# Performance work log

Hardware: AMD Instinct MI355X
Metric: run time of the kernel (lower is better)

Reference implementation:

```python
import jax, jax.numpy as jnp
import numpy as np

N_TOK = 16384   # total tokens (batch*seq)
H = 2048        # hidden_size
I = 768         # moe_intermediate_size (per-expert MLP width)
TOPK = 8        # num_experts_per_tok


def setup_inputs() -> dict:
    key = jax.random.key(0)
    ks = jax.random.split(key, 7)
    hidden_states = jax.random.normal(ks[0], (N_TOK, H), dtype=jnp.float32)
    # expert_mask[j, k] != 0 means token k selected this expert at top-k slot j
    expert_mask = jax.random.randint(ks[1], (TOPK, N_TOK), 0, 2, dtype=jnp.int32)
    routing_weights = jax.random.uniform(ks[2], (N_TOK, TOPK), dtype=jnp.float32)
    final_hidden_states = jax.random.normal(ks[3], (N_TOK, H), dtype=jnp.float32)
    gate_w = jax.random.normal(ks[4], (I, H), dtype=jnp.float32) * 0.02
    up_w = jax.random.normal(ks[5], (I, H), dtype=jnp.float32) * 0.02
    down_w = jax.random.normal(ks[6], (H, I), dtype=jnp.float32) * 0.02
    return {
        "hidden_states": hidden_states,
        "expert_mask": expert_mask,
        "routing_weights": routing_weights,
        "final_hidden_states": final_hidden_states,
        "gate_w": gate_w,
        "up_w": up_w,
        "down_w": down_w,
    }


def reference(hidden_states, expert_mask, routing_weights, final_hidden_states,
              gate_w, up_w, down_w):
    # forward_expert: gather selected tokens, SwiGLU MLP, scale by routing weight,
    # scatter-add into final_hidden_states. Equivalent jit-friendly form: the
    # combined routing weight per token is w[k] = sum_j mask[j,k]*routing_weights[k,j]
    # (tokens selected multiple times are summed, matching index_add_ semantics),
    # and unselected tokens get w[k]=0 so they contribute nothing.
    g = hidden_states @ gate_w.T                       # [N, I]
    u = hidden_states @ up_w.T                         # [N, I]
    y = (jax.nn.silu(g) * u) @ down_w.T                # [N, H]
    w = jnp.einsum('jk,kj->k', expert_mask.astype(y.dtype), routing_weights)  # [N]
    return final_hidden_states + y * w[:, None]
```

## Files before the change

### kernel.cpp

```cpp
#include <hip/hip_runtime.h>
#include <stdint.h>

#define NTOK 16384
#define HD   2048
#define ID   768
#define TOPK 8

typedef __bf16 bf16x8 __attribute__((ext_vector_type(8)));
typedef float  floatx4 __attribute__((ext_vector_type(4)));
typedef unsigned short ushort8 __attribute__((ext_vector_type(8)));

__device__ __forceinline__ unsigned short f32_to_bf16_rne(float f) {
    union { float f; uint32_t u; } v; v.f = f;
    uint32_t u = v.u;
    u += 0x7FFFu + ((u >> 16) & 1u);
    return (unsigned short)(u >> 16);
}
__device__ __forceinline__ float bf16_to_f32(unsigned short h) {
    union { uint32_t u; float f; } v; v.u = ((uint32_t)h) << 16;
    return v.f;
}

#define GLD_LDS(gsrc, ldst)                                                              \
    __builtin_amdgcn_global_load_lds(                                                    \
        (const __attribute__((address_space(1))) uint32_t*)(const void*)(gsrc),          \
        (__attribute__((address_space(3))) uint32_t*)(void*)(ldst), 16, 0, 0)

template<int VM> __device__ __forceinline__ void wait_vm() {
    if constexpr (VM == 4)      asm volatile("s_waitcnt vmcnt(4)" ::: "memory");
    else                        asm volatile("s_waitcnt vmcnt(0)" ::: "memory");
}
#define BARRIER() do { asm volatile("" ::: "memory");              \
                       __builtin_amdgcn_s_barrier();               \
                       asm volatile("" ::: "memory"); } while (0)

__global__ __launch_bounds__(256) void compute_w_kernel(const int* __restrict__ mask,
                                                        const float* __restrict__ rw,
                                                        float* __restrict__ w) {
    int k = blockIdx.x * 256 + threadIdx.x;
    if (k >= NTOK) return;
    float acc = 0.f;
#pragma unroll
    for (int j = 0; j < TOPK; ++j)
        acc += (float)mask[j * NTOK + k] * rw[k * TOPK + j];
    w[k] = acc;
}

__global__ __launch_bounds__(256) void convert_hs_kernel(const float* __restrict__ src,
                                                         unsigned short* __restrict__ dst) {
    size_t i = (size_t)blockIdx.x * 256 + threadIdx.x;
    const float4* s = (const float4*)src;
    float4 a = s[2 * i], b = s[2 * i + 1];
    ushort8 o;
    o[0] = f32_to_bf16_rne(a.x); o[1] = f32_to_bf16_rne(a.y);
    o[2] = f32_to_bf16_rne(a.z); o[3] = f32_to_bf16_rne(a.w);
    o[4] = f32_to_bf16_rne(b.x); o[5] = f32_to_bf16_rne(b.y);
    o[6] = f32_to_bf16_rne(b.z); o[7] = f32_to_bf16_rne(b.w);
    *(ushort8*)(dst + 8 * i) = o;
}

__global__ __launch_bounds__(256) void convert_w3_kernel(const float* __restrict__ g,
                                                         const float* __restrict__ u,
                                                         const float* __restrict__ d,
                                                         unsigned short* __restrict__ dst) {
    const int per = ID * HD / 8;
    int i = blockIdx.x * 256 + threadIdx.x;
    int which = i / per;
    int off = i - which * per;
    const float* src = (which == 0) ? g : ((which == 1) ? u : d);
    const float4* s = (const float4*)src;
    float4 a = s[2 * (size_t)off], b = s[2 * (size_t)off + 1];
    ushort8 o;
    o[0] = f32_to_bf16_rne(a.x); o[1] = f32_to_bf16_rne(a.y);
    o[2] = f32_to_bf16_rne(a.z); o[3] = f32_to_bf16_rne(a.w);
    o[4] = f32_to_bf16_rne(b.x); o[5] = f32_to_bf16_rne(b.y);
    o[6] = f32_to_bf16_rne(b.z); o[7] = f32_to_bf16_rne(b.w);
    *(ushort8*)(dst + 8 * (size_t)i) = o;
}

__global__ __launch_bounds__(256) void swiglu_kernel(const unsigned short* __restrict__ gu,
                                                     unsigned short* __restrict__ act) {
    int i = blockIdx.x * 256 + threadIdx.x;
    int t = i / (ID / 8);
    int c8 = i - t * (ID / 8);
    ushort8 g = *(const ushort8*)&gu[(size_t)t * (2 * ID) + c8 * 8];
    ushort8 u = *(const ushort8*)&gu[(size_t)t * (2 * ID) + ID + c8 * 8];
    ushort8 o;
#pragma unroll
    for (int j = 0; j < 8; ++j) {
        float gf = bf16_to_f32(g[j]);
        float uf = bf16_to_f32(u[j]);
        float s = gf / (1.f + __expf(-gf)) * uf;
        o[j] = f32_to_bf16_rne(s);
    }
    *(ushort8*)&act[(size_t)t * ID + c8 * 8] = o;
}

template<int K, int NC, bool FUSE_DOWN>
__global__ __launch_bounds__(512, 2) void gemm8p_kernel(
    const unsigned short* __restrict__ A,
    const unsigned short* __restrict__ B,
    unsigned short* __restrict__ Cb,
    const float* __restrict__ fin,
    const float* __restrict__ wtok,
    float* __restrict__ Cf) {
    constexpr int NT = K / 64;
    static_assert(NT >= 2, "");
    __shared__ __align__(16) unsigned short lds[2][4][8192];

    const int bid = blockIdx.x, nwg = gridDim.x;
    const int nb = (bid & 7) * (nwg >> 3) + (bid >> 3);
    const int bx = nb >> 6, by = nb & 63;
    const int row0 = by * 256, col0 = bx * 256;

    const int tid = threadIdx.x, wid = tid >> 6, lane = tid & 63;
    const int wr = wid >> 2, wc = wid & 3;
    const int lrow = lane & 15, q = lane >> 4;
    const int rsw = (((lrow >> 1) & 3) ^ q) << 4;

    const int srow = wid * 16 + (lane >> 2);
    const int kswz = (((lane & 3) ^ ((lane >> 3) & 3)) << 3);
    const unsigned short* sA0 = A + (size_t)(row0 + srow) * K + kswz;
    const unsigned short* sA1 = A + (size_t)(row0 + 128 + srow) * K + kswz;
    const unsigned short* sB0 = B + (size_t)(col0 + srow) * K + kswz;
    const unsigned short* sB1 = B + (size_t)(col0 + 128 + srow) * K + kswz;

#define STAGE(sb, reg, p0, p1, koff) do {                                   \
        GLD_LDS((p0) + (koff), &lds[sb][reg][wid * 512]);                   \
        GLD_LDS((p1) + (koff), &lds[sb][reg][4096 + wid * 512]);            \
    } while (0)

#define READ_A(ks) do { const unsigned short* rgn = &lds[s][(ks) * 2][0];   \
        _Pragma("unroll")                                                   \
        for (int m = 0; m < 8; ++m) {                                       \
            const int rl = wr * 128 + m * 16 + lrow;                        \
            af[m] = *(const bf16x8*)((const char*)rgn + rl * 64 + rsw);     \
        } } while (0)

#define READ_B(ks, nh) do { const unsigned short* rgn = &lds[s][(ks) * 2 + 1][0]; \
        _Pragma("unroll")                                                   \
        for (int n = 0; n < 2; ++n) {                                       \
            const int rl = wc * 64 + (nh) * 32 + n * 16 + lrow;             \
            bb[n] = *(const bf16x8*)((const char*)rgn + rl * 64 + rsw);     \
        } } while (0)

#define MFMA_Q(nh) do {                                                     \
        __builtin_amdgcn_s_setprio(1);                                      \
        _Pragma("unroll")                                                   \
        for (int m = 0; m < 8; ++m) {                                       \
            acc[m][(nh) * 2 + 0] = __builtin_amdgcn_mfma_f32_16x16x32_bf16(af[m], bb[0], acc[m][(nh) * 2 + 0], 0, 0, 0); \
            acc[m][(nh) * 2 + 1] = __builtin_amdgcn_mfma_f32_16x16x32_bf16(af[m], bb[1], acc[m][(nh) * 2 + 1], 0, 0, 0); \
        }                                                                   \
        __builtin_amdgcn_s_setprio(0);                                      \
    } while (0)

    floatx4 acc[8][4];
#pragma unroll
    for (int m = 0; m < 8; ++m)
#pragma unroll
        for (int n = 0; n < 4; ++n) acc[m][n] = (floatx4){0.f, 0.f, 0.f, 0.f};
    bf16x8 af[8], bb[2];

    STAGE(0, 0, sA0, sA1, 0);
    STAGE(0, 1, sB0, sB1, 0);
    STAGE(0, 2, sA0, sA1, 32);
    STAGE(0, 3, sB0, sB1, 32);
    wait_vm<4>();
    BARRIER();

    for (int t = 0; t < NT - 1; ++t) {
        const int s = t & 1, sn = s ^ 1;
        const int ko = (t + 1) * 64;
        READ_A(0); READ_B(0, 0);
        STAGE(sn, 0, sA0, sA1, ko);
        MFMA_Q(0);
        BARRIER();
        READ_B(0, 1);
        STAGE(sn, 1, sB0, sB1, ko);
        MFMA_Q(1);
        wait_vm<4>();
        BARRIER();
        READ_A(1); READ_B(1, 0);
        STAGE(sn, 2, sA0, sA1, ko + 32);
        MFMA_Q(0);
        BARRIER();
        READ_B(1, 1);
        STAGE(sn, 3, sB0, sB1, ko + 32);
        MFMA_Q(1);
        wait_vm<4>();
        BARRIER();
    }
    {
        const int s = (NT - 1) & 1;
        READ_A(0); READ_B(0, 0); MFMA_Q(0); BARRIER();
        READ_B(0, 1); MFMA_Q(1);
        wait_vm<0>();
        BARRIER();
        READ_A(1); READ_B(1, 0); MFMA_Q(0); BARRIER();
        READ_B(1, 1); MFMA_Q(1);
    }
#undef STAGE
#undef READ_A
#undef READ_B
#undef MFMA_Q

    if constexpr (!FUSE_DOWN) {
#pragma unroll
        for (int m = 0; m < 8; ++m)
#pragma unroll
            for (int r = 0; r < 4; ++r) {
                const int row = row0 + wr * 128 + m * 16 + q * 4 + r;
#pragma unroll
                for (int n = 0; n < 4; ++n) {
                    const int col = col0 + wc * 64 + n * 16 + lrow;
                    Cb[(size_t)row * NC + col] = f32_to_bf16_rne(acc[m][n][r]);
                }
            }
    } else {
#pragma unroll
        for (int m = 0; m < 8; ++m)
#pragma unroll
            for (int r = 0; r < 4; ++r) {
                const int row = row0 + wr * 128 + m * 16 + q * 4 + r;
                const float wv = wtok[row];
#pragma unroll
                for (int n = 0; n < 4; ++n) {
                    const int col = col0 + wc * 64 + n * 16 + lrow;
                    Cf[(size_t)row * NC + col] = fin[(size_t)row * NC + col] + wv * acc[m][n][r];
                }
            }
    }
}

extern "C" void kernel_launch(void* const* d_in, const int* in_sizes, int n_in,
                              void* d_out, int out_size, void* d_ws, size_t ws_size,
                              hipStream_t stream) {
    const float* hs   = (const float*)d_in[0];
    const int*   mask = (const int*)d_in[1];
    const float* rw   = (const float*)d_in[2];
    const float* fin  = (const float*)d_in[3];
    const float* gw   = (const float*)d_in[4];
    const float* uw   = (const float*)d_in[5];
    const float* dw   = (const float*)d_in[6];
    float* out = (float*)d_out;

    char* ws = (char*)d_ws;
    unsigned short* hs_b   = (unsigned short*)ws; ws += (size_t)NTOK * HD * 2;
    unsigned short* wcat_b = (unsigned short*)ws; ws += (size_t)3 * ID * HD * 2;
    unsigned short* gu_b   = (unsigned short*)ws; ws += (size_t)NTOK * 2 * ID * 2;
    float* wtok = (float*)ws;
    unsigned short* act_b = hs_b;
    unsigned short* down_b = wcat_b + (size_t)2 * ID * HD;

    compute_w_kernel<<<NTOK / 256, 256, 0, stream>>>(mask, rw, wtok);
    convert_hs_kernel<<<(NTOK * HD / 8) / 256, 256, 0, stream>>>(hs, hs_b);
    convert_w3_kernel<<<(3 * ID * HD / 8) / 256, 256, 0, stream>>>(gw, uw, dw, wcat_b);

    gemm8p_kernel<HD, 2 * ID, false><<<(NTOK / 256) * (2 * ID / 256), 512, 0, stream>>>(
        hs_b, wcat_b, gu_b, nullptr, nullptr, nullptr);

    swiglu_kernel<<<(NTOK * (ID / 8)) / 256, 256, 0, stream>>>(gu_b, act_b);

    gemm8p_kernel<ID, HD, true><<<(NTOK / 256) * (HD / 256), 512, 0, stream>>>(
        act_b, down_b, nullptr, fin, wtok, out);
}
```

Before: 259.0 us.

## Add dedicated 256x192-tile gate/up GEMM kernel with one block per CU

Replaces the generic 256x256-tile GEMM for the gate/up projection with a specialised kernel using 256x192 tiles, giving 512 workgroups (64 row tiles by 8 column tiles) instead of 384. It splits each 64-wide K step into two 32-wide halves, staged into double-buffered LDS with finer-grained waits so MFMA work overlaps the global-to-LDS loads. The aim is better wave quantisation across the CUs and better latency hiding. In exchange it runs at one block per CU with about 112KB of LDS, and writes the output with scalar bf16 stores.

```diff
diff --git a/kernel.cpp b/kernel.cpp
--- a/kernel.cpp
+++ b/kernel.cpp
@@ -28,6 +28,7 @@
 
 template<int VM> __device__ __forceinline__ void wait_vm() {
     if constexpr (VM == 4)      asm volatile("s_waitcnt vmcnt(4)" ::: "memory");
+    else if constexpr (VM == 3) asm volatile("s_waitcnt vmcnt(3)" ::: "memory");
     else                        asm volatile("s_waitcnt vmcnt(0)" ::: "memory");
 }
 #define BARRIER() do { asm volatile("" ::: "memory");              \
@@ -96,6 +97,136 @@
     *(ushort8*)&act[(size_t)t * ID + c8 * 8] = o;
 }
 
+__global__ __launch_bounds__(512, 1) void gemm_gu_kernel(
+    const unsigned short* __restrict__ A,
+    const unsigned short* __restrict__ B,
+    unsigned short* __restrict__ Cb) {
+    constexpr int K = HD;
+    constexpr int NT = K / 64;
+    __shared__ __align__(16) unsigned char lds[2][57344];
+
+    const int bid = blockIdx.x, nwg = gridDim.x;
+    const int nb = (bid & 7) * (nwg >> 3) + (bid >> 3);
+    const int bx = nb & 7, by = nb >> 3;
+    const int row0 = by * 256, col0 = bx * 192;
+
+    const int tid = threadIdx.x, wid = tid >> 6, lane = tid & 63;
+    const int wr = wid >> 2, wc = wid & 3;
+    const int lrow = lane & 15, q = lane >> 4;
+    const int rsw = ((q ^ ((lrow >> 1) & 3)) << 4);
+
+    const int kswz = (((lane & 3) ^ ((lane >> 3) & 3)) << 3);
+    const unsigned short* sA[2];
+#pragma unroll
+    for (int h = 0; h < 2; ++h) {
+        const int o = h * 8192 + wid * 1024 + lane * 16;
+        sA[h] = A + (size_t)(row0 + (o >> 6)) * K + kswz;
+    }
+    const unsigned short* sB[3];
+#pragma unroll
+    for (int r = 0; r < 3; ++r) {
+        const int o = r * 8192 + tid * 16;
+        const int ks = (o >= 12288) ? 1 : 0;
+        const int brow = (o - ks * 12288) >> 6;
+        sB[r] = B + (size_t)(col0 + brow) * K + ks * 32 + kswz;
+    }
+
+#define STAGE_A(sb, ks, kt) do {                                                            \
+        GLD_LDS(sA[0] + (kt) * 64 + (ks) * 32, lds[sb] + (ks) * 16384 + wid * 1024);        \
+        GLD_LDS(sA[1] + (kt) * 64 + (ks) * 32, lds[sb] + (ks) * 16384 + 8192 + wid * 1024); \
+    } while (0)
+#define STAGE_B01(sb, kt) do {                                                              \
+        GLD_LDS(sB[0] + (kt) * 64, lds[sb] + 32768 + wid * 1024);                           \
+        GLD_LDS(sB[1] + (kt) * 64, lds[sb] + 32768 + 8192 + wid * 1024);                    \
+    } while (0)
+#define STAGE_B2(sb, kt)                                                                    \
+        GLD_LDS(sB[2] + (kt) * 64, lds[sb] + 32768 + 16384 + wid * 1024)
+
+#define READ_A(s, ks) do { const unsigned char* rgn = lds[s] + (ks) * 16384;                \
+        _Pragma("unroll")                                                                   \
+        for (int m = 0; m < 8; ++m)                                                         \
+            af[m] = *(const bf16x8*)(rgn + (wr * 128 + m * 16 + lrow) * 64 + rsw);          \
+    } while (0)
+#define READ_B(s, ks) do { const unsigned char* rgn = lds[s] + 32768 + (ks) * 12288;        \
+        _Pragma("unroll")                                                                   \
+        for (int n = 0; n < 3; ++n)                                                         \
+            bb[n] = *(const bf16x8*)(rgn + (wc * 48 + n * 16 + lrow) * 64 + rsw);           \
+    } while (0)
+#define MFMA_H(mh) do {                                                                     \
+        __builtin_amdgcn_s_setprio(1);                                                      \
+        _Pragma("unroll")                                                                   \
+        for (int m = (mh) * 4; m < (mh) * 4 + 4; ++m)                                       \
+            _Pragma("unroll")                                                               \
+            for (int n = 0; n < 3; ++n)                                                     \
+                acc[m][n] = __builtin_amdgcn_mfma_f32_16x16x32_bf16(af[m], bb[n], acc[m][n], 0, 0, 0); \
+        __builtin_amdgcn_s_setprio(0);                                                      \
+    } while (0)
+
+    floatx4 acc[8][3];
+#pragma unroll
+    for (int m = 0; m < 8; ++m)
+#pragma unroll
+        for (int n = 0; n < 3; ++n) acc[m][n] = (floatx4){0.f, 0.f, 0.f, 0.f};
+    bf16x8 af[8], bb[3];
+
+    STAGE_A(0, 0, 0);
+    STAGE_B01(0, 0);
+    STAGE_A(0, 1, 0);
+    STAGE_B2(0, 0);
+    wait_vm<3>();
+    BARRIER();
+
+    for (int t = 0; t < NT - 1; ++t) {
+        const int s = t & 1, sn = s ^ 1;
+        READ_A(s, 0); READ_B(s, 0);
+        STAGE_A(sn, 0, t + 1);
+        MFMA_H(0);
+        BARRIER();
+        STAGE_B01(sn, t + 1);
+        MFMA_H(1);
+        wait_vm<4>();
+        BARRIER();
+        READ_A(s, 1); READ_B(s, 1);
+        STAGE_A(sn, 1, t + 1);
+        MFMA_H(0);
+        BARRIER();
+        STAGE_B2(sn, t + 1);
+        MFMA_H(1);
+        wait_vm<3>();
+        BARRIER();
+    }
+    {
+        const int s = (NT - 1) & 1;
+        READ_A(s, 0); READ_B(s, 0);
+        MFMA_H(0);
+        BARRIER();
+        MFMA_H(1);
+        wait_vm<0>();
+        BARRIER();
+        READ_A(s, 1); READ_B(s, 1);
+        MFMA_H(0);
+        MFMA_H(1);
+    }
+#undef STAGE_A
+#undef STAGE_B01
+#undef STAGE_B2
+#undef READ_A
+#undef READ_B
+#undef MFMA_H
+
+#pragma unroll
+    for (int m = 0; m < 8; ++m)
+#pragma unroll
+        for (int r = 0; r < 4; ++r) {
+            const int row = row0 + wr * 128 + m * 16 + q * 4 + r;
+#pragma unroll
+            for (int n = 0; n < 3; ++n) {
+                const int col = col0 + wc * 48 + n * 16 + lrow;
+                Cb[(size_t)row * (2 * ID) + col] = f32_to_bf16_rne(acc[m][n][r]);
+            }
+        }
+}
+
 template<int K, int NC, bool FUSE_DOWN>
 __global__ __launch_bounds__(512, 2) void gemm8p_kernel(
     const unsigned short* __restrict__ A,
@@ -256,8 +387,7 @@
     convert_hs_kernel<<<(NTOK * HD / 8) / 256, 256, 0, stream>>>(hs, hs_b);
     convert_w3_kernel<<<(3 * ID * HD / 8) / 256, 256, 0, stream>>>(gw, uw, dw, wcat_b);
 
-    gemm8p_kernel<HD, 2 * ID, false><<<(NTOK / 256) * (2 * ID / 256), 512, 0, stream>>>(
-        hs_b, wcat_b, gu_b, nullptr, nullptr, nullptr);
+    gemm_gu_kernel<<<512, 512, 0, stream>>>(hs_b, wcat_b, gu_b);
 
     swiglu_kernel<<<(NTOK * (ID / 8)) / 256, 256, 0, stream>>>(gu_b, act_b);
 
```

Result: faster. 243.2 us (-6.1%).
